# Optimization experiments

Measured on AMD Instinct MI355X. Metric: run time of the kernel, lower is better.

Reference implementation:

```python
import jax, jax.numpy as jnp
import numpy as np

B, CHAR_LEN, LSTM, VOCAB, NATTN = 4096, 64, 400, 73, 10

def _lstm_cell(x, h, c, W_ih, W_hh, b):
    # gates: [B, 4*LSTM] in (i, f, g, o) order, matching torch.nn.LSTMCell
    g = x @ W_ih.T + h @ W_hh.T + b
    i, f, gg, o = jnp.split(g, 4, axis=1)
    i = jax.nn.sigmoid(i); f = jax.nn.sigmoid(f)
    gg = jnp.tanh(gg); o = jax.nn.sigmoid(o)
    c_new = f * c + i * gg
    h_new = o * jnp.tanh(c_new)
    return h_new, c_new

def setup_inputs() -> dict:
    key = jax.random.key(0)
    ks = jax.random.split(key, 24)
    d = {}
    d['inputs'] = jax.random.normal(ks[0], (B, 3), jnp.float32)
    for n, k in zip(['h1','c1','h2','c2','h3','c3'], ks[1:7]):
        d[n] = jax.random.normal(k, (B, LSTM), jnp.float32) * 0.1
    d['kappa'] = jax.random.uniform(ks[7], (B, NATTN), jnp.float32) * 5.0
    d['w_prev'] = jax.random.uniform(ks[8], (B, VOCAB), jnp.float32)
    d['attention_values'] = jax.random.uniform(ks[9], (B, CHAR_LEN, VOCAB), jnp.float32)
    d['attention_lengths'] = jax.random.randint(ks[10], (B,), 1, CHAR_LEN + 1, jnp.int32)
    s = 0.05
    in1 = VOCAB + 3              # lstm1 input: [w, inputs]
    in23 = 3 + LSTM + VOCAB      # lstm2/3 input: [inputs, h, w]
    attn_in = VOCAB + 3 + LSTM
    d['W_ih1'] = jax.random.normal(ks[11], (4 * LSTM, in1), jnp.float32) * s
    d['W_hh1'] = jax.random.normal(ks[12], (4 * LSTM, LSTM), jnp.float32) * s
    d['b1'] = jax.random.normal(ks[13], (4 * LSTM,), jnp.float32) * s
    d['W_attn'] = jax.random.normal(ks[14], (3 * NATTN, attn_in), jnp.float32) * s
    d['b_attn'] = jax.random.normal(ks[15], (3 * NATTN,), jnp.float32) * s
    d['W_ih2'] = jax.random.normal(ks[16], (4 * LSTM, in23), jnp.float32) * s
    d['W_hh2'] = jax.random.normal(ks[17], (4 * LSTM, LSTM), jnp.float32) * s
    d['b2'] = jax.random.normal(ks[18], (4 * LSTM,), jnp.float32) * s
    d['W_ih3'] = jax.random.normal(ks[19], (4 * LSTM, in23), jnp.float32) * s
    d['W_hh3'] = jax.random.normal(ks[20], (4 * LSTM, LSTM), jnp.float32) * s
    d['b3'] = jax.random.normal(ks[21], (4 * LSTM,), jnp.float32) * s
    return d

def reference(inputs, h1, c1, h2, c2, h3, c3, kappa, w_prev, attention_values,
              attention_lengths, W_ih1, W_hh1, b1, W_attn, b_attn,
              W_ih2, W_hh2, b2, W_ih3, W_hh3, b3):
    char_len = attention_values.shape[1]
    # --- LSTM 1 ---
    s1_in = jnp.concatenate([w_prev, inputs], axis=1)
    h1n, c1n = _lstm_cell(s1_in, h1, c1, W_ih1, W_hh1, b1)
    # --- Gaussian-mixture location attention ---
    attn_in = jnp.concatenate([w_prev, inputs, h1n], axis=1)
    attn_params = jax.nn.softplus(attn_in @ W_attn.T + b_attn)
    alpha, beta, kap = jnp.split(attn_params, 3, axis=1)
    kap = kappa + kap / 25.0
    beta = jnp.maximum(beta, 0.01)
    u = jnp.arange(char_len, dtype=jnp.float32)[None, None, :]           # [1,1,C]
    phi = jnp.sum(alpha[:, :, None] *
                  jnp.exp(-jnp.square(kap[:, :, None] - u) / beta[:, :, None]),
                  axis=1)                                                 # [B,C]
    seq_mask = (jnp.arange(char_len)[None, :] < attention_lengths[:, None]).astype(jnp.float32)
    w = jnp.einsum('bc,bcv->bv', phi * seq_mask, attention_values)        # [B,V]
    # --- LSTM 2 & 3 ---
    s2_in = jnp.concatenate([inputs, h1n, w], axis=1)
    h2n, c2n = _lstm_cell(s2_in, h2, c2, W_ih2, W_hh2, b2)
    s3_in = jnp.concatenate([inputs, h2n, w], axis=1)
    h3n, c3n = _lstm_cell(s3_in, h3, c3, W_ih3, W_hh3, b3)
    return h3n
```

## Files before the change

kernel.cpp:

```cpp
#include <hip/hip_runtime.h>
#include <hip/hip_bf16.h>


#define B_SZ     4096
#define LSTM_N   400
#define NG       1600
#define VOCAB    73
#define NATTN    10
#define CHARLEN  64
#define KP1      512
#define KP23     896

typedef _Float16 half8 __attribute__((ext_vector_type(8)));
typedef __attribute__((ext_vector_type(4))) float floatx4;

__device__ __forceinline__ void gload_lds16(const void* g, void* l) {
    __builtin_amdgcn_global_load_lds(
        (const __attribute__((address_space(1))) void*)g,
        (__attribute__((address_space(3))) void*)l, 16, 0, 0);
}

__device__ __forceinline__ int lds_off(int r, int g) {
    return (r << 6) + ((((g ^ r) & 7)) << 3);
}

#define CW1   102400
#define CW23  179200
#define CWA   4096
#define CX1   262144
#define CXA   57344
#define CX23  253952
#define O1    (CW1)
#define O2    (O1 + CW23)
#define O3    (O2 + CW23)
#define O4    (O3 + CWA)
#define O5    (O4 + CX1)
#define O6    (O5 + CXA)
#define O7    (O6 + CX23)

__global__ __launch_bounds__(256) void pack_all(const float* __restrict__ Wih1,
                                                const float* __restrict__ Whh1,
                                                const float* __restrict__ Wih2,
                                                const float* __restrict__ Whh2,
                                                const float* __restrict__ Wih3,
                                                const float* __restrict__ Whh3,
                                                const float* __restrict__ W_attn,
                                                const float* __restrict__ w_prev,
                                                const float* __restrict__ inputs,
                                                const float* __restrict__ h1,
                                                const float* __restrict__ h2,
                                                const float* __restrict__ h3,
                                                _Float16* __restrict__ W1,
                                                _Float16* __restrict__ W2,
                                                _Float16* __restrict__ W3,
                                                _Float16* __restrict__ Wa,
                                                _Float16* __restrict__ X1,
                                                _Float16* __restrict__ XA,
                                                _Float16* __restrict__ X2,
                                                _Float16* __restrict__ X3)
{
    const int id = blockIdx.x * 256 + threadIdx.x;
    half8 hv;

    if (id < O1) {
        const int row = id >> 6;
        const int k0  = (id & 63) << 3;
        const int u = row >> 2, g = row & 3;
        const int src = g * 400 + u;
#pragma unroll
        for (int e = 0; e < 8; e++) {
            const int k = k0 + e;
            float x = 0.f;
            if (k < 76)           x = Wih1[(size_t)src * 76 + k];
            else if (k < 476)     x = Whh1[(size_t)src * 400 + (k - 76)];
            hv[e] = (_Float16)x;
        }
        *(half8*)(W1 + (size_t)row * KP1 + k0) = hv;
    } else if (id < O3) {
        const int id2 = id - O1;
        const bool is3 = (id2 >= CW23);
        const int id3 = is3 ? id2 - CW23 : id2;
        const int row = id3 / 112;
        const int k0  = (id3 - row * 112) << 3;
        const int u = row >> 2, g = row & 3;
        const int src = g * 400 + u;
        const float* Wih = is3 ? Wih3 : Wih2;
        const float* Whh = is3 ? Whh3 : Whh2;
#pragma unroll
        for (int e = 0; e < 8; e++) {
            const int k = k0 + e;
            float x = 0.f;
            if (k < 400)          x = Wih[(size_t)src * 476 + 3 + k];
            else if (k < 403)     x = Wih[(size_t)src * 476 + (k - 400)];
            else if (k < 476)     x = Wih[(size_t)src * 476 + k];
            else if (k < 876)     x = Whh[(size_t)src * 400 + (k - 476)];
            hv[e] = (_Float16)x;
        }
        *(half8*)((is3 ? W3 : W2) + (size_t)row * KP23 + k0) = hv;
    } else if (id < O4) {
        const int id4 = id - O3;
        const int row = id4 >> 6;
        const int k0  = (id4 & 63) << 3;
#pragma unroll
        for (int e = 0; e < 8; e++) {
            const int k = k0 + e;
            float x = 0.f;
            if (row < 30) {
                if (k < 400)      x = W_attn[(size_t)row * 476 + 76 + k];
                else if (k < 473) x = W_attn[(size_t)row * 476 + (k - 400)];
                else if (k < 476) x = W_attn[(size_t)row * 476 + 73 + (k - 473)];
            }
            hv[e] = (_Float16)x;
        }
        *(half8*)(Wa + (size_t)row * KP1 + k0) = hv;
    } else if (id < O5) {
        const int id5 = id - O4;
        const int b  = id5 >> 6;
        const int k0 = (id5 & 63) << 3;
#pragma unroll
        for (int e = 0; e < 8; e++) {
            const int k = k0 + e;
            float x = 0.f;
            if (k < 73)           x = w_prev[(size_t)b * 73 + k];
            else if (k < 76)      x = inputs[(size_t)b * 3 + (k - 73)];
            else if (k < 476)     x = h1[(size_t)b * 400 + (k - 76)];
            hv[e] = (_Float16)x;
        }
        *(half8*)(X1 + (size_t)b * KP1 + k0) = hv;
    } else if (id < O6) {
        const int id6 = id - O5;
        const int b  = id6 / 14;
        const int k0 = 400 + ((id6 - b * 14) << 3);
#pragma unroll
        for (int e = 0; e < 8; e++) {
            const int k = k0 + e;
            float x = 0.f;
            if (k < 473)          x = w_prev[(size_t)b * 73 + (k - 400)];
            else if (k < 476)     x = inputs[(size_t)b * 3 + (k - 473)];
            hv[e] = (_Float16)x;
        }
        *(half8*)(XA + (size_t)b * KP1 + k0) = hv;
    } else if (id < O7) {
        const int id7 = id - O6;
        const int b  = id7 / 62;
        const int k0 = 400 + ((id7 - b * 62) << 3);
        half8 h2v, h3v;
#pragma unroll
        for (int e = 0; e < 8; e++) {
            const int k = k0 + e;
            float x2 = 0.f, x3 = 0.f;
            if (k < 403)                    { x2 = inputs[(size_t)b * 3 + (k - 400)]; x3 = x2; }
            else if (k >= 476 && k < 876)   { x2 = h2[(size_t)b * 400 + (k - 476)];
                                              x3 = h3[(size_t)b * 400 + (k - 476)]; }
            h2v[e] = (_Float16)x2;
            h3v[e] = (_Float16)x3;
        }
        *(half8*)(X2 + (size_t)b * KP23 + k0) = h2v;
        *(half8*)(X3 + (size_t)b * KP23 + k0) = h3v;
    }
}

template<int KP>
__global__ __launch_bounds__(512, 4) void gemm_fused_t(const _Float16* __restrict__ Wm,
                                                       const _Float16* __restrict__ X,
                                                       const float* __restrict__ bias,
                                                       const float* __restrict__ c_in,
                                                       _Float16* __restrict__ d1, int ld1,
                                                       _Float16* __restrict__ d2, int ld2,
                                                       float* __restrict__ fout)
{
    __shared__ _Float16 lds[2][320 * 64];

    const int t    = threadIdx.x;
    const int w    = t >> 6;
    const int lane = t & 63;
    const int quad = lane >> 4;
    const int l16  = lane & 15;
    const int fid  = blockIdx.y * 16 + blockIdx.x;
    const int xcd  = fid & 7;
    const int loc  = fid >> 3;
    const int bx   = xcd * 2 + loc / 25;
    const int by   = loc % 25;
    const int m0   = by * 64;
    const int n0   = bx * 256;
    const int wm   = (w >> 2) * 32;
    const int wn   = (w & 3) * 64;
    const int lr   = lane >> 3;
    const int gq   = (lane & 7) ^ lr;

    floatx4 acc[2][4] = {};

    auto stage = [&](int sb, int k0) {
        gload_lds16(Wm + (size_t)(m0 + w * 8 + lr) * KP + k0 + gq * 8,
                    &lds[sb][(w * 8) * 64]);
#pragma unroll
        for (int s = 0; s < 4; s++)
            gload_lds16(X + (size_t)(n0 + w * 32 + s * 8 + lr) * KP + k0 + gq * 8,
                        &lds[sb][(64 + w * 32 + s * 8) * 64]);
    };

    stage(0, 0);
    constexpr int NT = KP / 64;
#pragma unroll
    for (int kt = 0; kt < NT; kt++) {
        const int sb = kt & 1;
        if (kt + 1 < NT) {
            stage(sb ^ 1, (kt + 1) * 64);
            asm volatile("s_waitcnt vmcnt(5)" ::: "memory");
        } else {
            asm volatile("s_waitcnt vmcnt(0)" ::: "memory");
        }
        __builtin_amdgcn_s_barrier();
        __builtin_amdgcn_sched_barrier(0);

#pragma unroll
        for (int h = 0; h < 2; h++) {
            half8 af[2], bf[4];
#pragma unroll
            for (int i = 0; i < 2; i++)
                af[i] = *(const half8*)(&lds[sb][lds_off(wm + i * 16 + l16, h * 4 + quad)]);
#pragma unroll
            for (int i = 0; i < 4; i++)
                bf[i] = *(const half8*)(&lds[sb][lds_off(64 + wn + i * 16 + l16, h * 4 + quad)]);
            __builtin_amdgcn_s_setprio(1);
#pragma unroll
            for (int mt = 0; mt < 2; mt++)
#pragma unroll
                for (int nt = 0; nt < 4; nt++)
                    acc[mt][nt] = __builtin_amdgcn_mfma_f32_16x16x32_f16(
                        af[mt], bf[nt], acc[mt][nt], 0, 0, 0);
            __builtin_amdgcn_s_setprio(0);
        }
        __builtin_amdgcn_s_barrier();
    }
    __builtin_amdgcn_sched_barrier(0);

    const int u0 = m0 >> 2;
    float*    Cs   = (float*)&lds[0][0];
    _Float16* Hs16 = (_Float16*)&lds[1][0];
    float*    Hs32 = (float*)&lds[1][0];
    {
        const int bl = t >> 1;
        const int j0 = (t & 1) * 2;
#pragma unroll
        for (int j = 0; j < 2; j++) {
            floatx4 cv = *(const floatx4*)(c_in + (size_t)(n0 + bl) * LSTM_N
                                           + u0 + (j0 + j) * 4);
            *(floatx4*)(Cs + bl * 20 + (j0 + j) * 4) = cv;
        }
    }
    __syncthreads();

#pragma unroll
    for (int mt = 0; mt < 2; mt++) {
        const int ul = (wm >> 2) + mt * 4 + quad;
        const int u  = u0 + ul;
        const float bi  = bias[u];
        const float bff = bias[400 + u];
        const float bg  = bias[800 + u];
        const float bo  = bias[1200 + u];
#pragma unroll
        for (int nt = 0; nt < 4; nt++) {
            const int bl = wn + nt * 16 + l16;
            float gi = acc[mt][nt][0] + bi;
            float gf = acc[mt][nt][1] + bff;
            float gg = acc[mt][nt][2] + bg;
            float go = acc[mt][nt][3] + bo;
            float si = 1.f / (1.f + expf(-gi));
            float sf = 1.f / (1.f + expf(-gf));
            float so = 1.f / (1.f + expf(-go));
            float cn = sf * Cs[bl * 20 + ul] + si * tanhf(gg);
            float h  = so * tanhf(cn);
            if (fout) Hs32[bl * 20 + ul] = h;
            else      Hs16[bl * 24 + ul] = (_Float16)h;
        }
    }
    __syncthreads();

    if (fout) {
        const int bl = t >> 1;
        const int p0 = (t & 1) * 2;
#pragma unroll
        for (int j = 0; j < 2; j++) {
            floatx4 hvv = *(const floatx4*)(Hs32 + bl * 20 + (p0 + j) * 4);
            *(floatx4*)(fout + (size_t)(n0 + bl) * LSTM_N + u0 + (p0 + j) * 4) = hvv;
        }
    } else {
        const int bl = t >> 1;
        const int p  = t & 1;
        half8 hvv = *(const half8*)(Hs16 + bl * 24 + p * 8);
        *(half8*)(d1 + (size_t)(n0 + bl) * ld1 + u0 + p * 8) = hvv;
        if (d2) *(half8*)(d2 + (size_t)(n0 + bl) * ld2 + u0 + p * 8) = hvv;
    }
}

__global__ __launch_bounds__(256) void attn_fused(const _Float16* __restrict__ Wa,
                                                  const _Float16* __restrict__ XA,
                                                  const float* __restrict__ b_attn,
                                                  const float* __restrict__ kappa,
                                                  const float* __restrict__ AV,
                                                  const int* __restrict__ alen,
                                                  _Float16* __restrict__ X2,
                                                  _Float16* __restrict__ X3)
{
    __shared__ _Float16 Wa_s[30 * KP1];
    __shared__ float prm[4][32];
    __shared__ float phi_s[4][CHARLEN];

    const int t = threadIdx.x;
#pragma unroll
    for (int i = 0; i < 8; i++) {
        const int idx = t + i * 256;
        if (idx < 1920) {
            const int row = idx >> 6;
            const int c8  = (idx & 63) << 3;
            *(half8*)(&Wa_s[row * KP1 + c8]) = *(const half8*)(Wa + (size_t)row * KP1 + c8);
        }
    }
    __syncthreads();

    const int wave = t >> 6;
    const int lane = t & 63;
    const int b = blockIdx.x * 4 + wave;

    half8 xa = *(const half8*)(XA + (size_t)b * KP1 + lane * 8);
    float xf[8];
#pragma unroll
    for (int e = 0; e < 8; e++) xf[e] = (float)xa[e];

    float myp = 0.f;
#pragma unroll
    for (int m = 0; m < 30; m++) {
        half8 wv = *(const half8*)(&Wa_s[m * KP1 + lane * 8]);
        float s = 0.f;
#pragma unroll
        for (int e = 0; e < 8; e++) s += (float)wv[e] * xf[e];
#pragma unroll
        for (int sh = 32; sh >= 1; sh >>= 1) s += __shfl_xor(s, sh, 64);
        if (lane == m) myp = s;
    }

    if (lane < 30) {
        float p  = myp + b_attn[lane];
        float sp = (p > 20.f) ? p : log1pf(expf(p));
        float v;
        if (lane < 10)      v = sp;
        else if (lane < 20) v = fmaxf(sp, 0.01f);
        else                v = kappa[(size_t)b * NATTN + (lane - 20)] + sp * (1.f / 25.f);
        prm[wave][lane] = v;
    }
    __syncthreads();

    const int len = alen[b];
    {
        int c = lane;
        float phi = 0.f;
#pragma unroll
        for (int j = 0; j < NATTN; j++) {
            float d = prm[wave][20 + j] - (float)c;
            phi += prm[wave][j] * expf(-d * d / prm[wave][10 + j]);
        }
        phi_s[wave][c] = (c < len) ? phi : 0.f;
    }
    __syncthreads();

    for (int v0 = 0; v0 < VOCAB; v0 += 64) {
        const int v = v0 + lane;
        if (v < VOCAB) {
            const float* avb = AV + (size_t)b * CHARLEN * VOCAB + v;
            float s = 0.f;
            for (int c = 0; c < len; c++)
                s += phi_s[wave][c] * avb[(size_t)c * VOCAB];
            _Float16 wv = (_Float16)s;
            X2[(size_t)b * KP23 + 403 + v] = wv;
            X3[(size_t)b * KP23 + 403 + v] = wv;
        }
    }
}

extern "C" void kernel_launch(void* const* d_in, const int* in_sizes, int n_in,
                              void* d_out, int out_size, void* d_ws, size_t ws_size,
                              hipStream_t stream)
{
    const float* inputs = (const float*)d_in[0];
    const float* h1     = (const float*)d_in[1];
    const float* c1     = (const float*)d_in[2];
    const float* h2     = (const float*)d_in[3];
    const float* c2     = (const float*)d_in[4];
    const float* h3     = (const float*)d_in[5];
    const float* c3     = (const float*)d_in[6];
    const float* kappa  = (const float*)d_in[7];
    const float* w_prev = (const float*)d_in[8];
    const float* AV     = (const float*)d_in[9];
    const int*   alen   = (const int*)d_in[10];
    const float* W_ih1  = (const float*)d_in[11];
    const float* W_hh1  = (const float*)d_in[12];
    const float* b1     = (const float*)d_in[13];
    const float* W_attn = (const float*)d_in[14];
    const float* b_attn = (const float*)d_in[15];
    const float* W_ih2  = (const float*)d_in[16];
    const float* W_hh2  = (const float*)d_in[17];
    const float* b2     = (const float*)d_in[18];
    const float* W_ih3  = (const float*)d_in[19];
    const float* W_hh3  = (const float*)d_in[20];
    const float* b3     = (const float*)d_in[21];
    float* out = (float*)d_out;

    char* p = (char*)d_ws;
    _Float16* X1 = (_Float16*)p; p += (size_t)B_SZ * KP1 * 2;
    _Float16* XA = (_Float16*)p; p += (size_t)B_SZ * KP1 * 2;
    _Float16* X2 = (_Float16*)p; p += (size_t)B_SZ * KP23 * 2;
    _Float16* X3 = (_Float16*)p; p += (size_t)B_SZ * KP23 * 2;
    _Float16* W1 = (_Float16*)p; p += (size_t)NG * KP1 * 2;
    _Float16* W2 = (_Float16*)p; p += (size_t)NG * KP23 * 2;
    _Float16* W3 = (_Float16*)p; p += (size_t)NG * KP23 * 2;
    _Float16* Wa = (_Float16*)p; p += (size_t)64 * KP1 * 2;

    pack_all<<<O7 / 256, 256, 0, stream>>>(W_ih1, W_hh1, W_ih2, W_hh2,
                                           W_ih3, W_hh3, W_attn,
                                           w_prev, inputs, h1, h2, h3,
                                           W1, W2, W3, Wa, X1, XA, X2, X3);

    const dim3 fgrid(16, 25);

    gemm_fused_t<KP1><<<fgrid, 512, 0, stream>>>(W1, X1, b1, c1,
                                                 XA, KP1, X2, KP23, nullptr);
    attn_fused<<<B_SZ / 4, 256, 0, stream>>>(Wa, XA, b_attn, kappa, AV, alen, X2, X3);
    gemm_fused_t<KP23><<<fgrid, 512, 0, stream>>>(W2, X2, b2, c2,
                                                  X3, KP23, nullptr, 0, nullptr);
    gemm_fused_t<KP23><<<fgrid, 512, 0, stream>>>(W3, X3, b3, c3,
                                                  nullptr, 0, nullptr, 0, out);
}
```

Baseline: 282.0 us.

## Halve GEMM K-tile to 32 and raise occupancy target to six blocks

The fused LSTM GEMM now stages K in chunks of 32 instead of 64, which halves shared memory per block. The launch-bounds occupancy hint rises from 4 to 6 blocks per CU. Staging is reorganised so each of the first four waves loads a 16-row slice of the weight tile, the XOR swizzle is dropped, and the per-wave vmcnt waits are adjusted. This trades more barriers and K iterations, plus possible LDS bank conflicts from the unswizzled layout, for higher occupancy and better latency hiding.

After: 292.0 us. +3.6%, slower.

```diff
diff --git a/kernel.cpp b/kernel.cpp
--- a/kernel.cpp
+++ b/kernel.cpp
@@ -18,10 +18,6 @@
     __builtin_amdgcn_global_load_lds(
         (const __attribute__((address_space(1))) void*)g,
         (__attribute__((address_space(3))) void*)l, 16, 0, 0);
-}
-
-__device__ __forceinline__ int lds_off(int r, int g) {
-    return (r << 6) + ((((g ^ r) & 7)) << 3);
 }
 
 #define CW1   102400
@@ -161,7 +157,7 @@
 }
 
 template<int KP>
-__global__ __launch_bounds__(512, 4) void gemm_fused_t(const _Float16* __restrict__ Wm,
+__global__ __launch_bounds__(512, 6) void gemm_fused_t(const _Float16* __restrict__ Wm,
                                                        const _Float16* __restrict__ X,
                                                        const float* __restrict__ bias,
                                                        const float* __restrict__ c_in,
@@ -169,7 +165,7 @@
                                                        _Float16* __restrict__ d2, int ld2,
                                                        float* __restrict__ fout)
 {
-    __shared__ _Float16 lds[2][320 * 64];
+    __shared__ _Float16 lds[2][320 * 32];
 
     const int t    = threadIdx.x;
     const int w    = t >> 6;
@@ -185,43 +181,51 @@
     const int n0   = bx * 256;
     const int wm   = (w >> 2) * 32;
     const int wn   = (w & 3) * 64;
-    const int lr   = lane >> 3;
-    const int gq   = (lane & 7) ^ lr;
+    const int lrow = lane >> 2;
+    const int lgr  = lane & 3;
 
     floatx4 acc[2][4] = {};
 
-    auto stage = [&](int sb, int k0) {
-        gload_lds16(Wm + (size_t)(m0 + w * 8 + lr) * KP + k0 + gq * 8,
-                    &lds[sb][(w * 8) * 64]);
-#pragma unroll
-        for (int s = 0; s < 4; s++)
-            gload_lds16(X + (size_t)(n0 + w * 32 + s * 8 + lr) * KP + k0 + gq * 8,
-                        &lds[sb][(64 + w * 32 + s * 8) * 64]);
+    auto stageB = [&](int sb, int k0) {
+#pragma unroll
+        for (int j = 0; j < 2; j++)
+            gload_lds16(X + (size_t)(n0 + w * 32 + j * 16 + lrow) * KP + k0 + lgr * 8,
+                        &lds[sb][(64 + w * 32 + j * 16) * 32]);
     };
-
-    stage(0, 0);
-    constexpr int NT = KP / 64;
+    auto stageA = [&](int sb, int k0) {
+        gload_lds16(Wm + (size_t)(m0 + w * 16 + lrow) * KP + k0 + lgr * 8,
+                    &lds[sb][(w * 16) * 32]);
+    };
+
+    if (w < 4) { stageA(0, 0); }
+    stageB(0, 0);
+    constexpr int NT = KP / 32;
 #pragma unroll
     for (int kt = 0; kt < NT; kt++) {
         const int sb = kt & 1;
         if (kt + 1 < NT) {
-            stage(sb ^ 1, (kt + 1) * 64);
-            asm volatile("s_waitcnt vmcnt(5)" ::: "memory");
+            if (w < 4) {
+                stageA(sb ^ 1, (kt + 1) * 32);
+                stageB(sb ^ 1, (kt + 1) * 32);
+                asm volatile("s_waitcnt vmcnt(3)" ::: "memory");
+            } else {
+                stageB(sb ^ 1, (kt + 1) * 32);
+                asm volatile("s_waitcnt vmcnt(2)" ::: "memory");
+            }
         } else {
             asm volatile("s_waitcnt vmcnt(0)" ::: "memory");
         }
         __builtin_amdgcn_s_barrier();
         __builtin_amdgcn_sched_barrier(0);
 
-#pragma unroll
-        for (int h = 0; h < 2; h++) {
+        {
             half8 af[2], bf[4];
 #pragma unroll
             for (int i = 0; i < 2; i++)
-                af[i] = *(const half8*)(&lds[sb][lds_off(wm + i * 16 + l16, h * 4 + quad)]);
+                af[i] = *(const half8*)(&lds[sb][(wm + i * 16 + l16) * 32 + quad * 8]);
 #pragma unroll
             for (int i = 0; i < 4; i++)
-                bf[i] = *(const half8*)(&lds[sb][lds_off(64 + wn + i * 16 + l16, h * 4 + quad)]);
+                bf[i] = *(const half8*)(&lds[sb][(64 + wn + i * 16 + l16) * 32 + quad * 8]);
             __builtin_amdgcn_s_setprio(1);
 #pragma unroll
             for (int mt = 0; mt < 2; mt++)
```
